# Performance work log

Measured on AMD Instinct MI355X. Metric: run time of the kernel, lower is better.

Reference implementation:

```python
import jax, jax.numpy as jnp
import numpy as np

H = 1024
V = 32000
S = 2048


def _lstm_cell(x, h_prev, c_prev, W_ih, W_hh, b_ih, b_hh):
    # PyTorch gate order: input, forget, cell(g), output
    gates = x @ W_ih.T + b_ih + h_prev @ W_hh.T + b_hh  # (1, 4H)
    i, f, g, o = jnp.split(gates, 4, axis=-1)
    i = jax.nn.sigmoid(i)
    f = jax.nn.sigmoid(f)
    g = jnp.tanh(g)
    o = jax.nn.sigmoid(o)
    c_new = f * c_prev + i * g
    h_new = o * jnp.tanh(c_new)
    return h_new, c_new


def setup_inputs() -> dict:
    key = jax.random.key(0)
    ks = jax.random.split(key, 16)
    sc = 0.05
    inp = {
        "input_ids": jax.random.randint(ks[0], (1,), 0, V, dtype=jnp.int64) if jax.config.jax_enable_x64 else jax.random.randint(ks[0], (1,), 0, V, dtype=jnp.int32),
        "h": jax.random.normal(ks[1], (2, 1, H), jnp.float32),
        "c": jax.random.normal(ks[2], (2, 1, H), jnp.float32),
        "encoder_outputs": jax.random.normal(ks[3], (S, H), jnp.float32),
        "embedding": jax.random.normal(ks[4], (V, H), jnp.float32) * sc,
        "W_ih0": jax.random.normal(ks[5], (4 * H, H), jnp.float32) * sc,
        "W_hh0": jax.random.normal(ks[6], (4 * H, H), jnp.float32) * sc,
        "b_ih0": jax.random.normal(ks[7], (4 * H,), jnp.float32) * sc,
        "b_hh0": jax.random.normal(ks[8], (4 * H,), jnp.float32) * sc,
        "W_ih1": jax.random.normal(ks[9], (4 * H, H), jnp.float32) * sc,
        "W_hh1": jax.random.normal(ks[10], (4 * H, H), jnp.float32) * sc,
        "b_ih1": jax.random.normal(ks[11], (4 * H,), jnp.float32) * sc,
        "b_hh1": jax.random.normal(ks[12], (4 * H,), jnp.float32) * sc,
        "W_out": jax.random.normal(ks[13], (V, H), jnp.float32) * sc,
        "b_out": jax.random.normal(ks[14], (V,), jnp.float32) * sc,
    }
    return inp


def reference(input_ids, h, c, encoder_outputs, embedding,
              W_ih0, W_hh0, b_ih0, b_hh0,
              W_ih1, W_hh1, b_ih1, b_hh1,
              W_out, b_out):
    # embedding lookup; dropout is identity in eval mode
    x = embedding[input_ids[0]][None, :]                      # (1, H)

    # attention: scores against layer-0 hidden state
    scores = encoder_outputs @ h[0, 0]                        # (S,)
    attn_w = jax.nn.softmax(scores)                           # (S,)
    ctx = attn_w @ encoder_outputs                            # (H,) attention_applied
    ctx_h = ctx[None, :]                                      # (1, H)

    # custom hidden-state injection: both layers' h replaced by context
    h0, c0 = _lstm_cell(x, ctx_h, c[0], W_ih0, W_hh0, b_ih0, b_hh0)
    h1, c1 = _lstm_cell(h0, ctx_h, c[1], W_ih1, W_hh1, b_ih1, b_hh1)

    logits = h1 @ W_out.T + b_out                             # (1, V)
    h_new = jnp.stack([h0, h1])                               # (2, 1, H)
    c_new = jnp.stack([c0, c1])                               # (2, 1, H)
    return logits, h_new, c_new, attn_w[None, :]
```

## Files before the change

### kernel.cpp

```cpp
#include <hip/hip_runtime.h>

#define HH 1024
#define VV 32000
#define SS 2048
#define TAG_MAGIC 0x13579BDFu

__device__ __forceinline__ float wave_sum64(float v) {
    #pragma unroll
    for (int off = 32; off; off >>= 1) v += __shfl_down(v, off, 64);
    return v;
}
__device__ __forceinline__ float fsigmoid(float x) { return 1.f / (1.f + __expf(-x)); }
__device__ __forceinline__ float ftanh(float x)    { return 1.f - 2.f / (__expf(2.f * x) + 1.f); }
__device__ __forceinline__ float dot4(float4 a, float4 b) {
    return a.x * b.x + a.y * b.y + a.z * b.z + a.w * b.w;
}
__device__ __forceinline__ float rowdot(const float4* Wr, int lane,
                                        float4 x0, float4 x1, float4 x2, float4 x3) {
    return dot4(Wr[lane], x0) + dot4(Wr[lane + 64], x1)
         + dot4(Wr[lane + 128], x2) + dot4(Wr[lane + 192], x3);
}

__device__ __forceinline__ void tag_store(unsigned long long* slot, float v) {
    unsigned long long p = ((unsigned long long)TAG_MAGIC << 32)
                         | (unsigned long long)__float_as_uint(v);
    __hip_atomic_store(slot, p, __ATOMIC_RELAXED, __HIP_MEMORY_SCOPE_AGENT);
}
__device__ __forceinline__ float tag_poll(unsigned long long* slot) {
    unsigned long long p = __hip_atomic_load(slot, __ATOMIC_RELAXED, __HIP_MEMORY_SCOPE_AGENT);
    while ((unsigned)(p >> 32) != TAG_MAGIC) {
        __builtin_amdgcn_s_sleep(1);
        p = __hip_atomic_load(slot, __ATOMIC_RELAXED, __HIP_MEMORY_SCOPE_AGENT);
    }
    return __uint_as_float((unsigned)p);
}

__global__ __launch_bounds__(256) void kA(
    const float* __restrict__ E, const float* __restrict__ h_in,
    const float* __restrict__ Wih0, const float* __restrict__ bih0,
    const float* __restrict__ bhh0,
    const float* __restrict__ emb, const int* __restrict__ ids,
    unsigned long long* __restrict__ scoreT, float* __restrict__ g0,
    float* __restrict__ ctx, float* __restrict__ attn_out)
{
    __shared__ float red[4];
    __shared__ float s_max, s_sum;
    __shared__ float wgt[16];
    const int tid = threadIdx.x, lane = tid & 63, warp = tid >> 6;
    const int gw = blockIdx.x * 4 + warp;
    if (blockIdx.x == 0) ((float4*)ctx)[tid] = make_float4(0.f, 0.f, 0.f, 0.f);

    {
        const float4* hv = (const float4*)h_in;
        float4 h0 = hv[lane], h1 = hv[lane + 64], h2 = hv[lane + 128], h3 = hv[lane + 192];
        float s = rowdot((const float4*)(E + (size_t)gw * HH), lane, h0, h1, h2, h3);
        s = wave_sum64(s);
        if (lane == 0) tag_store(&scoreT[gw], s);
    }
    {
        const float4* xv = (const float4*)(emb + (size_t)ids[0] * HH);
        float4 x0 = xv[lane], x1 = xv[lane + 64], x2 = xv[lane + 128], x3 = xv[lane + 192];
        #pragma unroll
        for (int t = 0; t < 2; ++t) {
            int row = gw + t * 2048;
            float a = rowdot((const float4*)(Wih0 + (size_t)row * HH), lane, x0, x1, x2, x3);
            a = wave_sum64(a);
            if (lane == 0) g0[row] = a + bih0[row] + bhh0[row];
        }
    }
    if (blockIdx.x >= 128) return;

    float va[4], vb[4];
    #pragma unroll
    for (int k = 0; k < 4; ++k) va[k] = tag_poll(&scoreT[4 * tid + k]);
    #pragma unroll
    for (int k = 0; k < 4; ++k) vb[k] = tag_poll(&scoreT[1024 + 4 * tid + k]);

    float m = fmaxf(fmaxf(fmaxf(va[0], va[1]), fmaxf(va[2], va[3])),
                    fmaxf(fmaxf(vb[0], vb[1]), fmaxf(vb[2], vb[3])));
    #pragma unroll
    for (int off = 32; off; off >>= 1) m = fmaxf(m, __shfl_xor(m, off, 64));
    if (lane == 0) red[warp] = m;
    __syncthreads();
    if (tid == 0) s_max = fmaxf(fmaxf(red[0], red[1]), fmaxf(red[2], red[3]));
    __syncthreads();
    float sm = s_max;
    float sum = 0.f;
    #pragma unroll
    for (int k = 0; k < 4; ++k) sum += __expf(va[k] - sm) + __expf(vb[k] - sm);
    sum = wave_sum64(sum);
    if (lane == 0) red[warp] = sum;
    __syncthreads();
    if (tid == 0) s_sum = red[0] + red[1] + red[2] + red[3];
    __syncthreads();
    float inv = 1.f / s_sum;
    int rowBase = blockIdx.x * 16;
    if (tid < 16) {
        float aw = __expf(tag_poll(&scoreT[rowBase + tid]) - sm) * inv;
        wgt[tid] = aw;
        attn_out[rowBase + tid] = aw;
    }
    __syncthreads();
    float4 acc = make_float4(0.f, 0.f, 0.f, 0.f);
    #pragma unroll
    for (int s = 0; s < 16; ++s) {
        float w = wgt[s];
        float4 e = ((const float4*)(E + (size_t)(rowBase + s) * HH))[tid];
        acc.x += w * e.x; acc.y += w * e.y; acc.z += w * e.z; acc.w += w * e.w;
    }
    atomicAdd(&ctx[4 * tid + 0], acc.x);
    atomicAdd(&ctx[4 * tid + 1], acc.y);
    atomicAdd(&ctx[4 * tid + 2], acc.z);
    atomicAdd(&ctx[4 * tid + 3], acc.w);
}

__global__ __launch_bounds__(256) void k3_whh(
    const float* __restrict__ Whh0, const float* __restrict__ Whh1,
    const float* __restrict__ bih1, const float* __restrict__ bhh1,
    const float* __restrict__ ctx, float* __restrict__ g0, float* __restrict__ g1) {
    int tid = threadIdx.x;
    int w = (blockIdx.x * 256 + tid) >> 6;
    int lane = tid & 63;
    const float4* cv = (const float4*)ctx;
    float4 c0 = cv[lane], c1 = cv[lane + 64], c2 = cv[lane + 128], c3 = cv[lane + 192];
    float a = rowdot((const float4*)(Whh0 + (size_t)w * HH), lane, c0, c1, c2, c3);
    a = wave_sum64(a);
    float b = rowdot((const float4*)(Whh1 + (size_t)w * HH), lane, c0, c1, c2, c3);
    b = wave_sum64(b);
    if (lane == 0) {
        g0[w] += a;
        g1[w] = b + bih1[w] + bhh1[w];
    }
}

__global__ __launch_bounds__(256) void k4_gates1(
    const float* __restrict__ Wih1, const float* __restrict__ g0,
    const float* __restrict__ c0_in, float* __restrict__ g1,
    float* __restrict__ h0_out, float* __restrict__ c0_out) {
    __shared__ float4 hs[256];
    int tid = threadIdx.x, warp = tid >> 6, lane = tid & 63;
    int row0 = blockIdx.x * 8 + warp * 2;
    const float4* Wr = (const float4*)(Wih1 + (size_t)row0 * HH);
    float4 a0 = Wr[lane], a1 = Wr[lane + 64], a2 = Wr[lane + 128], a3 = Wr[lane + 192];
    const float4* W2 = Wr + 256;
    float4 b0 = W2[lane], b1 = W2[lane + 64], b2 = W2[lane + 128], b3 = W2[lane + 192];
    {
        float4 gi = ((const float4*)(g0       ))[tid];
        float4 gf = ((const float4*)(g0 + 1024))[tid];
        float4 gg = ((const float4*)(g0 + 2048))[tid];
        float4 go = ((const float4*)(g0 + 3072))[tid];
        float4 cp = ((const float4*)c0_in)[tid];
        float4 c4, h4;
        c4.x = fsigmoid(gf.x) * cp.x + fsigmoid(gi.x) * ftanh(gg.x);
        c4.y = fsigmoid(gf.y) * cp.y + fsigmoid(gi.y) * ftanh(gg.y);
        c4.z = fsigmoid(gf.z) * cp.z + fsigmoid(gi.z) * ftanh(gg.z);
        c4.w = fsigmoid(gf.w) * cp.w + fsigmoid(gi.w) * ftanh(gg.w);
        h4.x = fsigmoid(go.x) * ftanh(c4.x);
        h4.y = fsigmoid(go.y) * ftanh(c4.y);
        h4.z = fsigmoid(go.z) * ftanh(c4.z);
        h4.w = fsigmoid(go.w) * ftanh(c4.w);
        hs[tid] = h4;
        if (blockIdx.x == 0) {
            ((float4*)h0_out)[tid] = h4;
            ((float4*)c0_out)[tid] = c4;
        }
    }
    __syncthreads();
    float4 x0 = hs[lane], x1 = hs[lane + 64], x2 = hs[lane + 128], x3 = hs[lane + 192];
    float acc0 = dot4(a0, x0) + dot4(a1, x1) + dot4(a2, x2) + dot4(a3, x3);
    acc0 = wave_sum64(acc0);
    if (lane == 0) g1[row0] += acc0;
    float acc1 = dot4(b0, x0) + dot4(b1, x1) + dot4(b2, x2) + dot4(b3, x3);
    acc1 = wave_sum64(acc1);
    if (lane == 0) g1[row0 + 1] += acc1;
}

__global__ __launch_bounds__(256) void k5_logits(
    const float* __restrict__ W, const float* __restrict__ bout,
    const float* __restrict__ g1, const float* __restrict__ c1_in,
    float* __restrict__ h1_out, float* __restrict__ c1_out,
    float* __restrict__ out) {
    __shared__ float4 hs[256];
    int tid = threadIdx.x, warp = tid >> 6, lane = tid & 63;
    int row0 = blockIdx.x * 32 + warp * 8;
    const float4* Wr = (const float4*)(W + (size_t)row0 * HH);
    float4 buf[2][4];
    buf[0][0] = Wr[lane];       buf[0][1] = Wr[lane + 64];
    buf[0][2] = Wr[lane + 128]; buf[0][3] = Wr[lane + 192];
    {
        const float4* N1 = Wr + 256;
        buf[1][0] = N1[lane];       buf[1][1] = N1[lane + 64];
        buf[1][2] = N1[lane + 128]; buf[1][3] = N1[lane + 192];
    }
    {
        float4 gi = ((const float4*)(g1       ))[tid];
        float4 gf = ((const float4*)(g1 + 1024))[tid];
        float4 gg = ((const float4*)(g1 + 2048))[tid];
        float4 go = ((const float4*)(g1 + 3072))[tid];
        float4 cp = ((const float4*)c1_in)[tid];
        float4 c4, h4;
        c4.x = fsigmoid(gf.x) * cp.x + fsigmoid(gi.x) * ftanh(gg.x);
        c4.y = fsigmoid(gf.y) * cp.y + fsigmoid(gi.y) * ftanh(gg.y);
        c4.z = fsigmoid(gf.z) * cp.z + fsigmoid(gi.z) * ftanh(gg.z);
        c4.w = fsigmoid(gf.w) * cp.w + fsigmoid(gi.w) * ftanh(gg.w);
        h4.x = fsigmoid(go.x) * ftanh(c4.x);
        h4.y = fsigmoid(go.y) * ftanh(c4.y);
        h4.z = fsigmoid(go.z) * ftanh(c4.z);
        h4.w = fsigmoid(go.w) * ftanh(c4.w);
        hs[tid] = h4;
        if (blockIdx.x == 0) {
            ((float4*)h1_out)[tid] = h4;
            ((float4*)c1_out)[tid] = c4;
        }
    }
    __syncthreads();
    float4 x0 = hs[lane], x1 = hs[lane + 64], x2 = hs[lane + 128], x3 = hs[lane + 192];
    #pragma unroll
    for (int i = 0; i < 8; ++i) {
        float acc = dot4(buf[i & 1][0], x0) + dot4(buf[i & 1][1], x1)
                  + dot4(buf[i & 1][2], x2) + dot4(buf[i & 1][3], x3);
        if (i + 2 < 8) {
            const float4* Nx = Wr + (i + 2) * 256;
            buf[i & 1][0] = Nx[lane];       buf[i & 1][1] = Nx[lane + 64];
            buf[i & 1][2] = Nx[lane + 128]; buf[i & 1][3] = Nx[lane + 192];
        }
        acc = wave_sum64(acc);
        if (lane == 0) out[row0 + i] = acc + bout[row0 + i];
    }
}

extern "C" void kernel_launch(void* const* d_in, const int* in_sizes, int n_in,
                              void* d_out, int out_size, void* d_ws, size_t ws_size,
                              hipStream_t stream) {
    const int*   ids   = (const int*)  d_in[0];
    const float* h_in  = (const float*)d_in[1];
    const float* c_in  = (const float*)d_in[2];
    const float* E     = (const float*)d_in[3];
    const float* emb   = (const float*)d_in[4];
    const float* Wih0  = (const float*)d_in[5];
    const float* Whh0  = (const float*)d_in[6];
    const float* bih0  = (const float*)d_in[7];
    const float* bhh0  = (const float*)d_in[8];
    const float* Wih1  = (const float*)d_in[9];
    const float* Whh1  = (const float*)d_in[10];
    const float* bih1  = (const float*)d_in[11];
    const float* bhh1  = (const float*)d_in[12];
    const float* Wout  = (const float*)d_in[13];
    const float* bout  = (const float*)d_in[14];

    float* out = (float*)d_out;
    float* logits   = out;
    float* h0_out   = out + 32000;
    float* h1_out   = out + 33024;
    float* c0_out   = out + 34048;
    float* c1_out   = out + 35072;
    float* attn_out = out + 36096;

    char* ws = (char*)d_ws;
    unsigned long long* scoreT = (unsigned long long*)(ws);
    float* ctx = (float*)(ws + 16384);
    float* g0  = (float*)(ws + 20480);
    float* g1  = (float*)(ws + 36864);

    kA<<<512, 256, 0, stream>>>(E, h_in, Wih0, bih0, bhh0, emb, ids,
                                scoreT, g0, ctx, attn_out);
    k3_whh<<<1024, 256, 0, stream>>>(Whh0, Whh1, bih1, bhh1, ctx, g0, g1);
    k4_gates1<<<512, 256, 0, stream>>>(Wih1, g0, c_in, g1, h0_out, c0_out);
    k5_logits<<<1000, 256, 0, stream>>>(Wout, bout, g1, c_in + 1024,
                                        h1_out, c1_out, logits);
}
```

Before: 57.53 us.

## Prefetch output projection weights into cache from earlier-stage kernels

Blocks in kA that would otherwise exit early, plus extra tail loops in k3_whh and k4_gates1, now stream disjoint slices of W_out through a dummy reduction. Together the slices cover nearly the whole matrix. The aim is to warm the large last-level cache with W_out while the latency-bound earlier stages run, so the final logits kernel reads mostly from cache instead of HBM. The cost is extra memory traffic and longer runtime in the earlier kernels. It also risks evicting data they need, or the prefetched lines being evicted before k5 runs.

```diff
diff --git a/kernel.cpp b/kernel.cpp
--- a/kernel.cpp
+++ b/kernel.cpp
@@ -35,11 +35,13 @@
     return __uint_as_float((unsigned)p);
 }
 
+
 __global__ __launch_bounds__(256) void kA(
     const float* __restrict__ E, const float* __restrict__ h_in,
     const float* __restrict__ Wih0, const float* __restrict__ bih0,
     const float* __restrict__ bhh0,
     const float* __restrict__ emb, const int* __restrict__ ids,
+    const float* __restrict__ Wout,
     unsigned long long* __restrict__ scoreT, float* __restrict__ g0,
     float* __restrict__ ctx, float* __restrict__ attn_out)
 {
@@ -68,7 +70,18 @@
             if (lane == 0) g0[row] = a + bih0[row] + bhh0[row];
         }
     }
-    if (blockIdx.x >= 128) return;
+    if (blockIdx.x >= 128) {
+        const float4* P = (const float4*)Wout;
+        const size_t pb = blockIdx.x - 128;
+        float dummy = 0.f;
+        #pragma unroll 4
+        for (int i = 0; i < 32; ++i) {
+            float4 v = P[(pb * 32 + i) * 256 + tid];
+            dummy += v.x + v.y + v.z + v.w;
+        }
+        asm volatile("" :: "v"(dummy));
+        return;
+    }
 
     float va[4], vb[4];
     #pragma unroll
@@ -117,7 +130,8 @@
 __global__ __launch_bounds__(256) void k3_whh(
     const float* __restrict__ Whh0, const float* __restrict__ Whh1,
     const float* __restrict__ bih1, const float* __restrict__ bhh1,
-    const float* __restrict__ ctx, float* __restrict__ g0, float* __restrict__ g1) {
+    const float* __restrict__ ctx, const float* __restrict__ Wout,
+    float* __restrict__ g0, float* __restrict__ g1) {
     int tid = threadIdx.x;
     int w = (blockIdx.x * 256 + tid) >> 6;
     int lane = tid & 63;
@@ -131,11 +145,22 @@
         g0[w] += a;
         g1[w] = b + bih1[w] + bhh1[w];
     }
+    {
+        const float4* P = (const float4*)Wout + 3145728;
+        float dummy = 0.f;
+        #pragma unroll 4
+        for (int i = 0; i < 12; ++i) {
+            float4 v = P[((size_t)blockIdx.x * 12 + i) * 256 + tid];
+            dummy += v.x + v.y + v.z + v.w;
+        }
+        asm volatile("" :: "v"(dummy));
+    }
 }
 
 __global__ __launch_bounds__(256) void k4_gates1(
     const float* __restrict__ Wih1, const float* __restrict__ g0,
-    const float* __restrict__ c0_in, float* __restrict__ g1,
+    const float* __restrict__ c0_in, const float* __restrict__ Wout,
+    float* __restrict__ g1,
     float* __restrict__ h0_out, float* __restrict__ c0_out) {
     __shared__ float4 hs[256];
     int tid = threadIdx.x, warp = tid >> 6, lane = tid & 63;
@@ -173,6 +198,16 @@
     float acc1 = dot4(b0, x0) + dot4(b1, x1) + dot4(b2, x2) + dot4(b3, x3);
     acc1 = wave_sum64(acc1);
     if (lane == 0) g1[row0 + 1] += acc1;
+    {
+        const float4* P = (const float4*)Wout + 6291456;
+        float dummy = 0.f;
+        #pragma unroll 2
+        for (int i = 0; i < 14; ++i) {
+            float4 v = P[((size_t)blockIdx.x * 14 + i) * 256 + tid];
+            dummy += v.x + v.y + v.z + v.w;
+        }
+        asm volatile("" :: "v"(dummy));
+    }
 }
 
 __global__ __launch_bounds__(256) void k5_logits(
@@ -262,10 +297,10 @@
     float* g0  = (float*)(ws + 20480);
     float* g1  = (float*)(ws + 36864);
 
-    kA<<<512, 256, 0, stream>>>(E, h_in, Wih0, bih0, bhh0, emb, ids,
+    kA<<<512, 256, 0, stream>>>(E, h_in, Wih0, bih0, bhh0, emb, ids, Wout,
                                 scoreT, g0, ctx, attn_out);
-    k3_whh<<<1024, 256, 0, stream>>>(Whh0, Whh1, bih1, bhh1, ctx, g0, g1);
-    k4_gates1<<<512, 256, 0, stream>>>(Wih1, g0, c_in, g1, h0_out, c0_out);
+    k3_whh<<<1024, 256, 0, stream>>>(Whh0, Whh1, bih1, bhh1, ctx, Wout, g0, g1);
+    k4_gates1<<<512, 256, 0, stream>>>(Wih1, g0, c_in, Wout, g1, h0_out, c0_out);
     k5_logits<<<1000, 256, 0, stream>>>(Wout, bout, g1, c_in + 1024,
                                         h1_out, c1_out, logits);
 }
```

Result: slower. 70.95 us (+23.3%).
